# Optimization experiments

Hardware: AMD Instinct MI355X
Metric: run time of the kernel (lower is better)

The kernel has to match this reference:

```python
import jax, jax.numpy as jnp
import numpy as np

B, N, H, W, NHOR = 4096, 128, 128, 64, 3

def setup_inputs() -> dict:
    key = jax.random.key(0)
    ks = jax.random.split(key, 11)
    s = 1.0 / np.sqrt(H)
    return {
        "embeddings": jax.random.normal(ks[0], (B, H), jnp.float32),
        "sensor_embeddings": jax.random.normal(ks[1], (B, N, H), jnp.float32),
        "sensor_logits": jax.random.normal(ks[2], (B, N), jnp.float32),
        "fc1_w": jax.random.normal(ks[3], (H, H), jnp.float32) * s,
        "fc1_b": jax.random.normal(ks[4], (H,), jnp.float32) * s,
        "fc2_w": jax.random.normal(ks[5], (NHOR * N, H), jnp.float32) * s,
        "fc2_b": jax.random.normal(ks[6], (NHOR * N,), jnp.float32) * s,
        "rw1": jax.random.normal(ks[7], (N, H, H), jnp.float32) * s,
        "rb1": jax.random.normal(ks[8], (N, H), jnp.float32) * s,
        "rw2": jax.random.normal(ks[9], (N, H, W), jnp.float32) * s,
        "rb2": jax.random.normal(ks[10], (N, W), jnp.float32) * s,
    }

def reference(embeddings, sensor_embeddings, sensor_logits,
              fc1_w, fc1_b, fc2_w, fc2_b, rw1, rb1, rw2, rb2):
    # Forecasting head: Linear -> ReLU -> (Dropout: identity in eval) -> Linear
    h = jax.nn.relu(embeddings @ fc1_w.T + fc1_b)              # (B, H)
    forecast = (h @ fc2_w.T + fc2_b).reshape(-1, NHOR, N)      # (B, NHOR, N)
    # Reconstruction heads: per-node MLPs batched as stacked GEMMs
    hn = jax.nn.relu(jnp.einsum('bnh,nhk->bnk', sensor_embeddings, rw1) + rb1)  # (B, N, H)
    recon = jnp.einsum('bnk,nkw->bnw', hn, rw2) + rb2          # (B, N, W)
    reconstruction = jnp.transpose(recon, (0, 2, 1))           # (B, W, N), matches torch.stack(dim=2)
    return (sensor_logits, forecast, reconstruction)
```

## Files before the change

### kernel.cpp

```cpp
#include <hip/hip_runtime.h>
#include <hip/hip_bf16.h>
#include <stdint.h>

typedef __attribute__((ext_vector_type(8))) short bf16x8;
typedef __attribute__((ext_vector_type(4))) float f32x4;

#define DEVI static __device__ __forceinline__

static constexpr int B_SZ = 4096, N_SZ = 128, H_SZ = 128, W_SZ = 64;

static constexpr size_t OFF_W1 = 0;
static constexpr size_t OFF_W2 = OFF_W1 + 4194304;
static constexpr size_t OFF_F1 = OFF_W2 + 2097152;
static constexpr size_t OFF_F2 = OFF_F1 + 32768;
static constexpr size_t OFF_H  = OFF_F2 + 98304;

DEVI unsigned short f2bf(float f) {
  union { __hip_bfloat16 b; unsigned short u; } cv;
  cv.b = __float2bfloat16(f);
  return cv.u;
}
DEVI float bf2f(unsigned short u) {
  union { unsigned int i; float f; } cv;
  cv.i = ((unsigned int)u) << 16;
  return cv.f;
}

DEVI void bar_lds() {
  __builtin_amdgcn_sched_barrier(0);
  asm volatile("s_waitcnt lgkmcnt(0)" ::: "memory");
  __builtin_amdgcn_s_barrier();
  __builtin_amdgcn_sched_barrier(0);
}

DEVI bf16x8 frag_ld(const unsigned char* base, int row, int kslot) {
  return *reinterpret_cast<const bf16x8*>(base + row * 256 + (((kslot ^ (row & 7)) << 4)));
}
DEVI bf16x8 gfrag_ld(const unsigned char* base, int row, int kslot) {
  return *reinterpret_cast<const bf16x8*>(base + row * 256 + (kslot << 4));
}

DEVI void stage_f32_tile(const float* src, int row_stride, unsigned char* dst, int tid, int nrows) {
  for (int t = tid; t < nrows * 16; t += 256) {
    int row = t >> 4, s = t & 15;
    const float* p = src + (size_t)row * row_stride + s * 8;
    union { unsigned short u[8]; uint4 v; } pk;
#pragma unroll
    for (int j = 0; j < 8; ++j) pk.u[j] = f2bf(p[j]);
    *reinterpret_cast<uint4*>(dst + row * 256 + ((s ^ (row & 7)) << 4)) = pk.v;
  }
}

__global__ __launch_bounds__(256) void prep_f1_kernel(const float* __restrict__ rw1,
                                                      const float* __restrict__ rw2,
                                                      const float* __restrict__ fc2w,
                                                      const float* __restrict__ slog,
                                                      const float* __restrict__ emb,
                                                      const float* __restrict__ fc1w,
                                                      const float* __restrict__ fc1b,
                                                      float* __restrict__ out,
                                                      unsigned char* __restrict__ ws) {
  __shared__ unsigned char sA[16384];
  __shared__ unsigned char sB[32768];

  const int bid = blockIdx.x;
  const int tid = threadIdx.x;
  if (bid < 2072) {
    const int T_W1 = 128 * 128 * 16;
    const int T_W2 = 128 * 64 * 16;
    const int T_F2 = 384 * 16;
    int id = bid * 256 + tid;
    if (id < T_W1) {
      int c = id & 127, rest = id >> 7;
      int s = rest & 15, n = rest >> 4;
      const float* src = rw1 + (size_t)n * 16384 + (size_t)(s * 8) * 128 + c;
      union { unsigned short u[8]; uint4 v; } pk;
#pragma unroll
      for (int j = 0; j < 8; ++j) pk.u[j] = f2bf(src[(size_t)j * 128]);
      size_t dst = OFF_W1 + ((size_t)n * 128 + c) * 256 + (size_t)(s << 4);
      *reinterpret_cast<uint4*>(ws + dst) = pk.v;
      return;
    }
    id -= T_W1;
    if (id < T_W2) {
      int w = id & 63, rest = id >> 6;
      int s = rest & 15, n = rest >> 4;
      const float* src = rw2 + (size_t)n * 8192 + (size_t)(s * 8) * 64 + w;
      union { unsigned short u[8]; uint4 v; } pk;
#pragma unroll
      for (int j = 0; j < 8; ++j) pk.u[j] = f2bf(src[(size_t)j * 64]);
      size_t dst = OFF_W2 + ((size_t)n * 64 + w) * 256 + (size_t)(s << 4);
      *reinterpret_cast<uint4*>(ws + dst) = pk.v;
      return;
    }
    id -= T_W2;
    if (id < T_F2) {
      int s = id & 15, o = id >> 4;
      const float* src = fc2w + (size_t)o * 128 + s * 8;
      union { unsigned short u[8]; uint4 v; } pk;
#pragma unroll
      for (int j = 0; j < 8; ++j) pk.u[j] = f2bf(src[j]);
      *reinterpret_cast<uint4*>(ws + OFF_F2 + (size_t)o * 256 + ((s ^ (o & 7)) << 4)) = pk.v;
      return;
    }
    id -= T_F2;
    reinterpret_cast<uint4*>(out)[id] = reinterpret_cast<const uint4*>(slog)[id];
    return;
  }

  const int bt = bid - 2072;
  const int b0 = bt * 64;
  stage_f32_tile(fc1w, 128, sB, tid, 128);
  stage_f32_tile(emb + (size_t)b0 * 128, 128, sA, tid, 64);
  __syncthreads();

  const int wave = tid >> 6, lane = tid & 63;
  const int wm = wave >> 1, wn = wave & 1;
  const int lr = lane & 15, lk = lane >> 4;

  f32x4 acc[2][4] = {};
#pragma unroll
  for (int kk = 0; kk < 4; ++kk) {
    const int slot = kk * 4 + lk;
    bf16x8 af[2], bfv[4];
#pragma unroll
    for (int m = 0; m < 2; ++m) af[m] = frag_ld(sA, wm * 32 + m * 16 + lr, slot);
#pragma unroll
    for (int q = 0; q < 4; ++q) bfv[q] = frag_ld(sB, wn * 64 + q * 16 + lr, slot);
#pragma unroll
    for (int m = 0; m < 2; ++m)
#pragma unroll
      for (int q = 0; q < 4; ++q)
        acc[m][q] = __builtin_amdgcn_mfma_f32_16x16x32_bf16(af[m], bfv[q], acc[m][q], 0, 0, 0);
  }

  unsigned char* tile = ws + OFF_H + (size_t)bt * 16384;
#pragma unroll
  for (int q = 0; q < 4; ++q) {
    int c = wn * 64 + q * 16 + lr;
    float bias = fc1b[c];
#pragma unroll
    for (int m = 0; m < 2; ++m) {
#pragma unroll
      for (int j = 0; j < 4; ++j) {
        int r = wm * 32 + m * 16 + lk * 4 + j;
        float v = acc[m][q][j] + bias;
        v = v > 0.f ? v : 0.f;
        *reinterpret_cast<unsigned short*>(tile + r * 256 + ((c * 2) ^ ((r & 7) << 4))) = f2bf(v);
      }
    }
  }
}

__global__ __launch_bounds__(256, 2) void recon_kernel(const float* __restrict__ se,
                                                       const float* __restrict__ rb1,
                                                       const float* __restrict__ rb2,
                                                       const unsigned char* __restrict__ ws,
                                                       float* __restrict__ out3) {
  __shared__ unsigned char smem[59136];

  const int bid = blockIdx.x;
  const int tid = threadIdx.x;
  const int wave = tid >> 6, lane = tid & 63;
  const int lr = lane & 15, lk = lane >> 4;

  unsigned char* sSE0 = smem;
  unsigned char* sSE1 = smem + 16384;
  unsigned char* sHN  = smem + 32768;
  unsigned char* sOUT = smem + 49152;
  float* sBIAS = reinterpret_cast<float*>(smem + 58368);

  const int n = bid & 127;
  const int btg = bid >> 7;
  const int b0 = btg * 512;

  const int wm = wave >> 1, wq = wave & 1;

  const unsigned char* w1b = ws + OFF_W1 + (size_t)n * 32768;
  const unsigned char* w2b = ws + OFF_W2 + (size_t)n * 16384;
  bf16x8 w1f[4][4];
#pragma unroll
  for (int m = 0; m < 4; ++m)
#pragma unroll
    for (int kk = 0; kk < 4; ++kk)
      w1f[m][kk] = gfrag_ld(w1b, wm * 64 + m * 16 + lr, kk * 4 + lk);

  if (tid < 192)
    sBIAS[tid] = (tid < 128) ? rb1[(size_t)n * 128 + tid] : rb2[(size_t)n * 64 + tid - 128];

  stage_f32_tile(se + ((size_t)b0 * 128 + n) * 128, 128 * 128, sSE0, tid, 64);
  unsigned short* outus = reinterpret_cast<unsigned short*>(out3);

  const int fb = tid >> 2, fqt = tid & 3;
  auto flush_out = [&](int tt) {
    uint4 v0 = *reinterpret_cast<const uint4*>(sOUT + fb * 144 + fqt * 32);
    uint4 v1 = *reinterpret_cast<const uint4*>(sOUT + fb * 144 + fqt * 32 + 16);
    unsigned short* dst = outus + (size_t)(b0 + tt * 64 + fb) * 16384 + 8192 + n * 64 + fqt * 16;
    *reinterpret_cast<uint4*>(dst) = v0;
    *reinterpret_cast<uint4*>(dst + 8) = v1;
  };

  float4 fra[4], frb[4];
  {
    const float* sb = se + ((size_t)(b0 + 64) * 128 + n) * 128;
#pragma unroll
    for (int k = 0; k < 4; ++k) {
      int c = tid + k * 256;
      int row = c >> 4, s = c & 15;
      const float* p = sb + (size_t)row * 16384 + s * 8;
      fra[k] = *reinterpret_cast<const float4*>(p);
      frb[k] = *reinterpret_cast<const float4*>(p + 4);
    }
  }
  bar_lds();

#pragma unroll 1
  for (int t = 0; t < 8; ++t) {
    unsigned char* bufc = (t & 1) ? sSE1 : sSE0;
    unsigned char* bufn = (t & 1) ? sSE0 : sSE1;

    f32x4 acc[4][2] = {};
#pragma unroll
    for (int kk = 0; kk < 4; ++kk) {
      const int slot = kk * 4 + lk;
      bf16x8 bv[2];
#pragma unroll
      for (int q = 0; q < 2; ++q) bv[q] = frag_ld(bufc, wq * 32 + q * 16 + lr, slot);
#pragma unroll
      for (int m = 0; m < 4; ++m)
#pragma unroll
        for (int q = 0; q < 2; ++q)
          acc[m][q] = __builtin_amdgcn_mfma_f32_16x16x32_bf16(w1f[m][kk], bv[q], acc[m][q], 0, 0, 0);
    }
    bar_lds();

    if (t > 0) flush_out(t - 1);

    if (t < 7) {
#pragma unroll
      for (int k = 0; k < 4; ++k) {
        int c = tid + k * 256;
        int row = c >> 4, s = c & 15;
        union { unsigned short u[8]; uint4 v; } pk;
#pragma unroll
        for (int j = 0; j < 4; ++j) pk.u[j] = f2bf(fra[k][j]);
#pragma unroll
        for (int j = 0; j < 4; ++j) pk.u[4 + j] = f2bf(frb[k][j]);
        *reinterpret_cast<uint4*>(bufn + row * 256 + ((s ^ (row & 7)) << 4)) = pk.v;
      }
    }
    if (t < 6) {
      const float* sb = se + ((size_t)(b0 + (t + 2) * 64) * 128 + n) * 128;
#pragma unroll
      for (int k = 0; k < 4; ++k) {
        int c = tid + k * 256;
        int row = c >> 4, s = c & 15;
        const float* p = sb + (size_t)row * 16384 + s * 8;
        fra[k] = *reinterpret_cast<const float4*>(p);
        frb[k] = *reinterpret_cast<const float4*>(p + 4);
      }
    }
    bf16x8 w2f[2][4];
#pragma unroll
    for (int m = 0; m < 2; ++m)
#pragma unroll
      for (int kk = 0; kk < 4; ++kk)
        w2f[m][kk] = gfrag_ld(w2b, wm * 32 + m * 16 + lr, kk * 4 + lk);

#pragma unroll
    for (int m = 0; m < 4; ++m) {
      const int k0 = wm * 64 + m * 16 + lk * 4;
      const int s16 = k0 >> 3, half = (k0 >> 2) & 1;
      union { float4 v; float f[4]; } b1;
      b1.v = *reinterpret_cast<const float4*>(sBIAS + k0);
#pragma unroll
      for (int q = 0; q < 2; ++q) {
        const int b = wq * 32 + q * 16 + lr;
        union { unsigned short u[4]; uint2 v; } pk;
#pragma unroll
        for (int j = 0; j < 4; ++j) {
          float v = acc[m][q][j] + b1.f[j];
          v = v > 0.f ? v : 0.f;
          pk.u[j] = f2bf(v);
        }
        *reinterpret_cast<uint2*>(sHN + b * 256 + ((s16 ^ (b & 7)) << 4) + half * 8) = pk.v;
      }
    }
    bar_lds();

    f32x4 acc2[2][2] = {};
#pragma unroll
    for (int kk = 0; kk < 4; ++kk) {
      const int slot = kk * 4 + lk;
      bf16x8 bv[2];
#pragma unroll
      for (int q = 0; q < 2; ++q) bv[q] = frag_ld(sHN, wq * 32 + q * 16 + lr, slot);
#pragma unroll
      for (int m = 0; m < 2; ++m)
#pragma unroll
        for (int q = 0; q < 2; ++q)
          acc2[m][q] = __builtin_amdgcn_mfma_f32_16x16x32_bf16(w2f[m][kk], bv[q], acc2[m][q], 0, 0, 0);
    }

#pragma unroll
    for (int m = 0; m < 2; ++m) {
      const int w0 = wm * 32 + m * 16 + lk * 4;
      union { float4 v; float f[4]; } b2;
      b2.v = *reinterpret_cast<const float4*>(sBIAS + 128 + w0);
#pragma unroll
      for (int q = 0; q < 2; ++q) {
        const int bloc = wq * 32 + q * 16 + lr;
        union { unsigned short u[4]; uint2 v; } pk;
#pragma unroll
        for (int j = 0; j < 4; ++j) pk.u[j] = f2bf(acc2[m][q][j] + b2.f[j]);
        *reinterpret_cast<uint2*>(sOUT + bloc * 144 + w0 * 2) = pk.v;
      }
    }
  }
  bar_lds();
  flush_out(7);
}

__global__ __launch_bounds__(256) void transpose_f2_kernel(float* __restrict__ out3,
                                                           const unsigned char* __restrict__ ws,
                                                           const float* __restrict__ fc2b,
                                                           float* __restrict__ out2) {
  __shared__ unsigned char smem[32768];
  const int bid = blockIdx.x;
  const int tid = threadIdx.x;
  const int wave = tid >> 6, lane = tid & 63;

  if (bid >= 4096) {
    const int fid = bid - 4096;
    const int bt = fid & 63, ch = fid >> 6;
    const int b0 = bt * 64;
    const int lr = lane & 15, lk = lane >> 4;
    unsigned char* sB = smem;
    {
      const uint4* bp = reinterpret_cast<const uint4*>(ws + OFF_F2 + (size_t)ch * 32768);
      uint4* db = reinterpret_cast<uint4*>(sB);
      for (int c = tid; c < 2048; c += 256) db[c] = bp[c];
    }
    __syncthreads();

    const int wm = wave >> 1, wn = wave & 1;
    const unsigned char* htile = ws + OFF_H + (size_t)bt * 16384;

    f32x4 acc[2][4] = {};
#pragma unroll
    for (int kk = 0; kk < 4; ++kk) {
      const int slot = kk * 4 + lk;
      bf16x8 af[2], bfv[4];
#pragma unroll
      for (int m = 0; m < 2; ++m) af[m] = frag_ld(htile, wm * 32 + m * 16 + lr, slot);
#pragma unroll
      for (int q = 0; q < 4; ++q) bfv[q] = frag_ld(sB, wn * 64 + q * 16 + lr, slot);
#pragma unroll
      for (int m = 0; m < 2; ++m)
#pragma unroll
        for (int q = 0; q < 4; ++q)
          acc[m][q] = __builtin_amdgcn_mfma_f32_16x16x32_bf16(af[m], bfv[q], acc[m][q], 0, 0, 0);
    }

#pragma unroll
    for (int q = 0; q < 4; ++q) {
      int o = ch * 128 + wn * 64 + q * 16 + lr;
      float bias = fc2b[o];
#pragma unroll
      for (int m = 0; m < 2; ++m) {
#pragma unroll
        for (int j = 0; j < 4; ++j) {
          int r = wm * 32 + m * 16 + lk * 4 + j;
          out2[(size_t)(b0 + r) * 384 + o] = acc[m][q][j] + bias;
        }
      }
    }
    return;
  }

  const int b = bid;
  const unsigned short* t = reinterpret_cast<const unsigned short*>(out3) + (size_t)b * 16384 + 8192;
  float* dst = out3 + (size_t)b * 8192;
  uint4 r[2][2];
#pragma unroll
  for (int half = 0; half < 2; ++half) {
    const int g = half * 4 + wave;
    r[half][0] = *reinterpret_cast<const uint4*>(t + lane * 64 + g * 8);
    r[half][1] = *reinterpret_cast<const uint4*>(t + (size_t)(lane + 64) * 64 + g * 8);
  }
  __syncthreads();
#pragma unroll
  for (int half = 0; half < 2; ++half) {
    const int g = half * 4 + wave;
    union { uint4 v; unsigned short u[8]; } p0, p1;
    p0.v = r[half][0];
    p1.v = r[half][1];
#pragma unroll
    for (int j = 0; j < 8; ++j) {
      dst[(g * 8 + j) * 128 + lane] = bf2f(p0.u[j]);
      dst[(g * 8 + j) * 128 + lane + 64] = bf2f(p1.u[j]);
    }
  }
}

extern "C" void kernel_launch(void* const* d_in, const int* in_sizes, int n_in,
                              void* d_out, int out_size, void* d_ws, size_t ws_size,
                              hipStream_t stream) {
  const float* emb  = (const float*)d_in[0];
  const float* se   = (const float*)d_in[1];
  const float* slog = (const float*)d_in[2];
  const float* fc1w = (const float*)d_in[3];
  const float* fc1b = (const float*)d_in[4];
  const float* fc2w = (const float*)d_in[5];
  const float* fc2b = (const float*)d_in[6];
  const float* rw1  = (const float*)d_in[7];
  const float* rb1  = (const float*)d_in[8];
  const float* rw2  = (const float*)d_in[9];
  const float* rb2  = (const float*)d_in[10];
  float* out = (float*)d_out;
  unsigned char* ws = (unsigned char*)d_ws;

  float* out2 = out + (size_t)B_SZ * N_SZ;
  float* out3 = out2 + (size_t)B_SZ * 384;

  prep_f1_kernel<<<2136, 256, 0, stream>>>(rw1, rw2, fc2w, slog, emb, fc1w, fc1b, out, ws);

  recon_kernel<<<1024, 256, 0, stream>>>(se, rb1, rb2, ws, out3);

  transpose_f2_kernel<<<4288, 256, 0, stream>>>(out3, ws, fc2b, out2);
}
```

Measured before the change: 136.7 us.

## Split recon_kernel work across 8 waves with 512-thread blocks

The recon kernel now runs 512 threads per block instead of 256, so each of 8 waves owns half as many output rows in both GEMMs. Per-thread register arrays for weights, accumulators and prefetch buffers shrink, and staging and flush work are spread over more threads. The aim is more wave-level parallelism to hide memory latency while the same 59 KB of LDS per block is kept. In exchange, the removed min-blocks hint may allow fewer blocks per CU, and each barrier now synchronizes more waves.

```diff
diff --git a/kernel.cpp b/kernel.cpp
--- a/kernel.cpp
+++ b/kernel.cpp
@@ -40,8 +40,9 @@
   return *reinterpret_cast<const bf16x8*>(base + row * 256 + (kslot << 4));
 }
 
+template <int NT>
 DEVI void stage_f32_tile(const float* src, int row_stride, unsigned char* dst, int tid, int nrows) {
-  for (int t = tid; t < nrows * 16; t += 256) {
+  for (int t = tid; t < nrows * 16; t += NT) {
     int row = t >> 4, s = t & 15;
     const float* p = src + (size_t)row * row_stride + s * 8;
     union { unsigned short u[8]; uint4 v; } pk;
@@ -110,8 +111,8 @@
 
   const int bt = bid - 2072;
   const int b0 = bt * 64;
-  stage_f32_tile(fc1w, 128, sB, tid, 128);
-  stage_f32_tile(emb + (size_t)b0 * 128, 128, sA, tid, 64);
+  stage_f32_tile<256>(fc1w, 128, sB, tid, 128);
+  stage_f32_tile<256>(emb + (size_t)b0 * 128, 128, sA, tid, 64);
   __syncthreads();
 
   const int wave = tid >> 6, lane = tid & 63;
@@ -152,11 +153,11 @@
   }
 }
 
-__global__ __launch_bounds__(256, 2) void recon_kernel(const float* __restrict__ se,
-                                                       const float* __restrict__ rb1,
-                                                       const float* __restrict__ rb2,
-                                                       const unsigned char* __restrict__ ws,
-                                                       float* __restrict__ out3) {
+__global__ __launch_bounds__(512) void recon_kernel(const float* __restrict__ se,
+                                                    const float* __restrict__ rb1,
+                                                    const float* __restrict__ rb2,
+                                                    const unsigned char* __restrict__ ws,
+                                                    float* __restrict__ out3) {
   __shared__ unsigned char smem[59136];
 
   const int bid = blockIdx.x;
@@ -174,38 +175,37 @@
   const int btg = bid >> 7;
   const int b0 = btg * 512;
 
-  const int wm = wave >> 1, wq = wave & 1;
+  const int wm = wave >> 1;
+  const int wq = wave & 1;
 
   const unsigned char* w1b = ws + OFF_W1 + (size_t)n * 32768;
   const unsigned char* w2b = ws + OFF_W2 + (size_t)n * 16384;
-  bf16x8 w1f[4][4];
-#pragma unroll
-  for (int m = 0; m < 4; ++m)
+  bf16x8 w1f[2][4];
+#pragma unroll
+  for (int m = 0; m < 2; ++m)
 #pragma unroll
     for (int kk = 0; kk < 4; ++kk)
-      w1f[m][kk] = gfrag_ld(w1b, wm * 64 + m * 16 + lr, kk * 4 + lk);
+      w1f[m][kk] = gfrag_ld(w1b, wm * 32 + m * 16 + lr, kk * 4 + lk);
 
   if (tid < 192)
     sBIAS[tid] = (tid < 128) ? rb1[(size_t)n * 128 + tid] : rb2[(size_t)n * 64 + tid - 128];
 
-  stage_f32_tile(se + ((size_t)b0 * 128 + n) * 128, 128 * 128, sSE0, tid, 64);
+  stage_f32_tile<512>(se + ((size_t)b0 * 128 + n) * 128, 128 * 128, sSE0, tid, 64);
   unsigned short* outus = reinterpret_cast<unsigned short*>(out3);
 
-  const int fb = tid >> 2, fqt = tid & 3;
+  const int fb = tid >> 3, fqt = tid & 7;
   auto flush_out = [&](int tt) {
-    uint4 v0 = *reinterpret_cast<const uint4*>(sOUT + fb * 144 + fqt * 32);
-    uint4 v1 = *reinterpret_cast<const uint4*>(sOUT + fb * 144 + fqt * 32 + 16);
-    unsigned short* dst = outus + (size_t)(b0 + tt * 64 + fb) * 16384 + 8192 + n * 64 + fqt * 16;
+    uint4 v0 = *reinterpret_cast<const uint4*>(sOUT + fb * 144 + fqt * 16);
+    unsigned short* dst = outus + (size_t)(b0 + tt * 64 + fb) * 16384 + 8192 + n * 64 + fqt * 8;
     *reinterpret_cast<uint4*>(dst) = v0;
-    *reinterpret_cast<uint4*>(dst + 8) = v1;
   };
 
-  float4 fra[4], frb[4];
+  float4 fra[2], frb[2];
   {
     const float* sb = se + ((size_t)(b0 + 64) * 128 + n) * 128;
 #pragma unroll
-    for (int k = 0; k < 4; ++k) {
-      int c = tid + k * 256;
+    for (int k = 0; k < 2; ++k) {
+      int c = tid + k * 512;
       int row = c >> 4, s = c & 15;
       const float* p = sb + (size_t)row * 16384 + s * 8;
       fra[k] = *reinterpret_cast<const float4*>(p);
@@ -219,7 +219,7 @@
     unsigned char* bufc = (t & 1) ? sSE1 : sSE0;
     unsigned char* bufn = (t & 1) ? sSE0 : sSE1;
 
-    f32x4 acc[4][2] = {};
+    f32x4 acc[2][2] = {};
 #pragma unroll
     for (int kk = 0; kk < 4; ++kk) {
       const int slot = kk * 4 + lk;
@@ -227,7 +227,7 @@
 #pragma unroll
       for (int q = 0; q < 2; ++q) bv[q] = frag_ld(bufc, wq * 32 + q * 16 + lr, slot);
 #pragma unroll
-      for (int m = 0; m < 4; ++m)
+      for (int m = 0; m < 2; ++m)
 #pragma unroll
         for (int q = 0; q < 2; ++q)
           acc[m][q] = __builtin_amdgcn_mfma_f32_16x16x32_bf16(w1f[m][kk], bv[q], acc[m][q], 0, 0, 0);
@@ -238,8 +238,8 @@
 
     if (t < 7) {
 #pragma unroll
-      for (int k = 0; k < 4; ++k) {
-        int c = tid + k * 256;
+      for (int k = 0; k < 2; ++k) {
+        int c = tid + k * 512;
         int row = c >> 4, s = c & 15;
         union { unsigned short u[8]; uint4 v; } pk;
 #pragma unroll
@@ -252,24 +252,22 @@
     if (t < 6) {
       const float* sb = se + ((size_t)(b0 + (t + 2) * 64) * 128 + n) * 128;
 #pragma unroll
-      for (int k = 0; k < 4; ++k) {
-        int c = tid + k * 256;
+      for (int k = 0; k < 2; ++k) {
+        int c = tid + k * 512;
         int row = c >> 4, s = c & 15;
         const float* p = sb + (size_t)row * 16384 + s * 8;
         fra[k] = *reinterpret_cast<const float4*>(p);
         frb[k] = *reinterpret_cast<const float4*>(p + 4);
       }
     }
-    bf16x8 w2f[2][4];
-#pragma unroll
-    for (int m = 0; m < 2; ++m)
-#pragma unroll
-      for (int kk = 0; kk < 4; ++kk)
-        w2f[m][kk] = gfrag_ld(w2b, wm * 32 + m * 16 + lr, kk * 4 + lk);
-
-#pragma unroll
-    for (int m = 0; m < 4; ++m) {
-      const int k0 = wm * 64 + m * 16 + lk * 4;
+    bf16x8 w2f[4];
+#pragma unroll
+    for (int kk = 0; kk < 4; ++kk)
+      w2f[kk] = gfrag_ld(w2b, wm * 16 + lr, kk * 4 + lk);
+
+#pragma unroll
+    for (int m = 0; m < 2; ++m) {
+      const int k0 = wm * 32 + m * 16 + lk * 4;
       const int s16 = k0 >> 3, half = (k0 >> 2) & 1;
       union { float4 v; float f[4]; } b1;
       b1.v = *reinterpret_cast<const float4*>(sBIAS + k0);
@@ -288,7 +286,7 @@
     }
     bar_lds();
 
-    f32x4 acc2[2][2] = {};
+    f32x4 acc2[2] = {};
 #pragma unroll
     for (int kk = 0; kk < 4; ++kk) {
       const int slot = kk * 4 + lk;
@@ -296,15 +294,12 @@
 #pragma unroll
       for (int q = 0; q < 2; ++q) bv[q] = frag_ld(sHN, wq * 32 + q * 16 + lr, slot);
 #pragma unroll
-      for (int m = 0; m < 2; ++m)
-#pragma unroll
-        for (int q = 0; q < 2; ++q)
-          acc2[m][q] = __builtin_amdgcn_mfma_f32_16x16x32_bf16(w2f[m][kk], bv[q], acc2[m][q], 0, 0, 0);
-    }
-
-#pragma unroll
-    for (int m = 0; m < 2; ++m) {
-      const int w0 = wm * 32 + m * 16 + lk * 4;
+      for (int q = 0; q < 2; ++q)
+        acc2[q] = __builtin_amdgcn_mfma_f32_16x16x32_bf16(w2f[kk], bv[q], acc2[q], 0, 0, 0);
+    }
+
+    {
+      const int w0 = wm * 16 + lk * 4;
       union { float4 v; float f[4]; } b2;
       b2.v = *reinterpret_cast<const float4*>(sBIAS + 128 + w0);
 #pragma unroll
@@ -312,7 +307,7 @@
         const int bloc = wq * 32 + q * 16 + lr;
         union { unsigned short u[4]; uint2 v; } pk;
 #pragma unroll
-        for (int j = 0; j < 4; ++j) pk.u[j] = f2bf(acc2[m][q][j] + b2.f[j]);
+        for (int j = 0; j < 4; ++j) pk.u[j] = f2bf(acc2[q][j] + b2.f[j]);
         *reinterpret_cast<uint2*>(sOUT + bloc * 144 + w0 * 2) = pk.v;
       }
     }
@@ -425,7 +420,7 @@
 
   prep_f1_kernel<<<2136, 256, 0, stream>>>(rw1, rw2, fc2w, slog, emb, fc1w, fc1b, out, ws);
 
-  recon_kernel<<<1024, 256, 0, stream>>>(se, rb1, rb2, ws, out3);
+  recon_kernel<<<1024, 512, 0, stream>>>(se, rb1, rb2, ws, out3);
 
   transpose_f2_kernel<<<4288, 256, 0, stream>>>(out3, ws, fc2b, out2);
 }
```

After: 130.5 us. 1.05x faster.
